# Kernel optimization log

Measured on AMD Instinct MI355X. Metric: run time of the kernel, lower is better.

The kernel has to match this reference:

```python
import jax, jax.numpy as jnp
import numpy as np

KERNEL = 3

def setup_inputs() -> dict:
    key = jax.random.key(0)
    k1, k2 = jax.random.split(key)
    x = jax.random.normal(k1, (32, 64, 64, 64), dtype=jnp.float32)
    weights = jax.random.normal(k2, (128, 64, KERNEL * KERNEL), dtype=jnp.float32)
    return {"x": x, "weights": weights}

def reference(x, weights):
    # x: (B, C, H, W); weights: (OC, C, k*k) with torch-unfold ordering
    # (channel slowest, kernel row-major) -> reshape to OIHW conv kernel.
    B, C, H, W = x.shape
    OC = weights.shape[0]
    wk = weights.reshape(OC, C, KERNEL, KERNEL)
    # stride-1, dilation-1, VALID conv == the unfold + per-(oc,c) matmul sum
    y = jax.lax.conv_general_dilated(
        x, wk, window_strides=(1, 1), padding="VALID",
        dimension_numbers=("NCHW", "OIHW", "NCHW"))
    Ho, Wo = y.shape[2], y.shape[3]
    # Faithful replication of the original's layout bug: results are laid out
    # as [oc*B + b] then reinterpreted via view(B, OC, Ho, Wo).
    y = jnp.transpose(y, (1, 0, 2, 3)).reshape(B, OC, Ho, Wo)
    return y
```

## Files before the change

kernel.cpp:

```cpp
#include <hip/hip_runtime.h>


typedef __attribute__((ext_vector_type(8))) short short8;
typedef __attribute__((ext_vector_type(4))) float f32x4;
typedef __attribute__((ext_vector_type(4))) unsigned int uint4v;

__device__ __forceinline__ unsigned short f2bf(float f) {
    unsigned u = __builtin_bit_cast(unsigned, f);
    u = (u + 0x7FFFu + ((u >> 16) & 1u)) >> 16;
    return (unsigned short)u;
}

__device__ __forceinline__ void glds16(const void* g, void* s) {
    __builtin_amdgcn_global_load_lds(
        (const __attribute__((address_space(1))) unsigned int*)g,
        (__attribute__((address_space(3))) unsigned int*)s, 16, 0, 0);
}

__global__ __launch_bounds__(256)
void transpose_x(const float* __restrict__ x, char* __restrict__ xT) {
    __shared__ float tile[64][65];
    const int tid = threadIdx.x;
    const int h = blockIdx.x, b = blockIdx.y;

    #pragma unroll
    for (int i = 0; i < 4; ++i) {
        const int idx = i * 256 + tid;
        const int c = idx >> 4, j = idx & 15;
        const float4 v = *(const float4*)(x + (size_t)(((b * 64 + c) * 64 + h) * 64 + j * 4));
        tile[c][j * 4 + 0] = v.x; tile[c][j * 4 + 1] = v.y;
        tile[c][j * 4 + 2] = v.z; tile[c][j * 4 + 3] = v.w;
    }
    __syncthreads();

    #pragma unroll
    for (int i = 0; i < 2; ++i) {
        const int idx = i * 256 + tid;
        const int col = idx >> 3, q = idx & 7;
        unsigned int wds[4];
        #pragma unroll
        for (int jj = 0; jj < 4; ++jj) {
            const unsigned short lo = f2bf(tile[q * 8 + 2 * jj + 0][col]);
            const unsigned short hi = f2bf(tile[q * 8 + 2 * jj + 1][col]);
            wds[jj] = (unsigned)lo | ((unsigned)hi << 16);
        }
        uint4v v; v[0] = wds[0]; v[1] = wds[1]; v[2] = wds[2]; v[3] = wds[3];
        *(uint4v*)(xT + (size_t)(((b * 64 + h) * 64 + col) * 128) + ((q ^ (col & 7)) * 16)) = v;
    }
}

__global__ __launch_bounds__(256)
void pack_w(const float* __restrict__ w, char* __restrict__ wT) {
    const int id = blockIdx.x * 256 + threadIdx.x;
    const int t = id >> 10;
    const int rem = id & 1023;
    const int oc = rem >> 3, q = rem & 7;
    unsigned int wds[4];
    #pragma unroll
    for (int jj = 0; jj < 4; ++jj) {
        const unsigned short lo = f2bf(w[(size_t)oc * 576 + (q * 8 + 2 * jj + 0) * 9 + t]);
        const unsigned short hi = f2bf(w[(size_t)oc * 576 + (q * 8 + 2 * jj + 1) * 9 + t]);
        wds[jj] = (unsigned)lo | ((unsigned)hi << 16);
    }
    uint4v v; v[0] = wds[0]; v[1] = wds[1]; v[2] = wds[2]; v[3] = wds[3];
    *(uint4v*)(wT + (size_t)(t * 16384 + oc * 128) + ((q ^ (oc & 7)) * 16)) = v;
}

__global__ __launch_bounds__(256, 2)
void quanv_mfma(const char* __restrict__ xT, const char* __restrict__ wT,
                float* __restrict__ out) {
    __shared__ __align__(16) char lds[65536];
    char* sx = lds;
    char* sw = lds + 49152;

    const int tid = threadIdx.x;
    const int lane = tid & 63;
    const int wid = tid >> 6;
    const int hot = blockIdx.x;
    const int b   = blockIdx.y;
    const int ho0 = hot * 4;

    for (int k = wid; k < 48; k += 4) {
        const int r = k >> 3, sub = k & 7;
        int gr = ho0 + r; if (gr > 63) gr = 63;
        glds16(xT + (size_t)((b * 64 + gr) * 8192 + sub * 1024 + lane * 16),
               sx + k * 1024);
    }
    for (int k = wid; k < 16; k += 4)
        glds16(wT + (size_t)(k * 1024 + lane * 16), sw + k * 1024);
    __syncthreads();

    const int l15 = lane & 15;
    const int quad = lane >> 4;
    const int r = wid;
    const int ho = ho0 + r;

    f32x4 acc[8][4];
    #pragma unroll
    for (int mt = 0; mt < 8; ++mt)
        #pragma unroll
        for (int nt = 0; nt < 4; ++nt)
            acc[mt][nt] = (f32x4){0.f, 0.f, 0.f, 0.f};

    #pragma unroll
    for (int tap = 0; tap < 9; ++tap) {
        const int kh = tap / 3, kw = tap % 3;

        uint4v pf[4];
        if (tap < 8) {
            #pragma unroll
            for (int i = 0; i < 4; ++i)
                pf[i] = *(const uint4v*)(wT + (size_t)((tap + 1) * 16384 +
                                                      (wid * 4 + i) * 1024 + lane * 16));
        }

        #pragma unroll
        for (int s = 0; s < 2; ++s) {
            const int q = s * 4 + quad;
            short8 a[8], bf[4];
            const int abase = l15 * 128 + ((q ^ (l15 & 7)) * 16);
            #pragma unroll
            for (int mt = 0; mt < 8; ++mt)
                a[mt] = *(const short8*)(sw + abase + mt * 2048);
            const int cb = kw + l15;
            const int bbase = (r + kh) * 8192 + cb * 128 + ((q ^ (cb & 7)) * 16);
            #pragma unroll
            for (int nt = 0; nt < 4; ++nt)
                bf[nt] = *(const short8*)(sx + bbase + nt * 2048);
            #pragma unroll
            for (int mt = 0; mt < 8; ++mt)
                #pragma unroll
                for (int nt = 0; nt < 4; ++nt)
                    acc[mt][nt] = __builtin_amdgcn_mfma_f32_16x16x32_bf16(
                        a[mt], bf[nt], acc[mt][nt], 0, 0, 0);
        }

        if (tap < 8) {
            __syncthreads();
            #pragma unroll
            for (int i = 0; i < 4; ++i)
                *(uint4v*)(sw + (wid * 4 + i) * 1024 + lane * 16) = pf[i];
            __syncthreads();
        }
    }

    if (ho < 62) {
        #pragma unroll
        for (int mt = 0; mt < 8; ++mt) {
            #pragma unroll
            for (int i = 0; i < 4; ++i) {
                const int oc = mt * 16 + quad * 4 + i;
                float* op = out + ((size_t)(oc * 32 + b) * 62 + ho) * 62;
                #pragma unroll
                for (int nt = 0; nt < 4; ++nt) {
                    const int wo = nt * 16 + l15;
                    if (wo < 62) op[wo] = acc[mt][nt][i];
                }
            }
        }
    }
}

#define CCH   8
#define OC_PT 8
#define ROWS  18
__global__ __launch_bounds__(256, 4)
void quanv_f32(const float* __restrict__ x, const float* __restrict__ w,
               float* __restrict__ out) {
    __shared__ float sx_raw[CCH * ROWS * 64 + 4];
    #define SX(cl, row, col) sx_raw[((cl) * ROWS + (row)) * 64 + (col)]
    const int tid = threadIdx.x;
    const int tx = tid & 15, ty = tid >> 4;
    const int hot = blockIdx.x, ocg = blockIdx.y, b = blockIdx.z;
    const int row0 = hot * 16, ho = row0 + ty, wo0 = tx * 4;
    const float* xb = x + (size_t)b * (64 * 64 * 64);
    const float* wb = w + (size_t)(ocg * OC_PT) * 576;
    float acc[OC_PT][4];
    #pragma unroll
    for (int o = 0; o < OC_PT; ++o)
        #pragma unroll
        for (int q = 0; q < 4; ++q) acc[o][q] = 0.f;
    for (int cc = 0; cc < 64; cc += CCH) {
        __syncthreads();
        #pragma unroll
        for (int j = 0; j < 9; ++j) {
            const int idx = j * 256 + tid;
            const int col4 = idx & 15, rowc = idx >> 4;
            const int row = rowc % ROWS, cl = rowc / ROWS;
            int gr = row0 + row; if (gr > 63) gr = 63;
            *(float4*)(&sx_raw[idx * 4]) =
                *(const float4*)(xb + ((size_t)(cc + cl) * 64 + gr) * 64 + col4 * 4);
        }
        __syncthreads();
        for (int cl = 0; cl < CCH; ++cl) {
            float xv[3][6];
            #pragma unroll
            for (int kh = 0; kh < 3; ++kh)
                #pragma unroll
                for (int j = 0; j < 6; ++j) xv[kh][j] = SX(cl, ty + kh, wo0 + j);
            const float* wc = wb + (size_t)(cc + cl) * 9;
            #pragma unroll
            for (int o = 0; o < OC_PT; ++o) {
                float wv[9];
                #pragma unroll
                for (int t = 0; t < 9; ++t) wv[t] = wc[(size_t)o * 576 + t];
                #pragma unroll
                for (int kh = 0; kh < 3; ++kh)
                    #pragma unroll
                    for (int kw = 0; kw < 3; ++kw) {
                        const float wvv = wv[kh * 3 + kw];
                        #pragma unroll
                        for (int q = 0; q < 4; ++q)
                            acc[o][q] = fmaf(xv[kh][kw + q], wvv, acc[o][q]);
                    }
            }
        }
    }
    if (ho < 62) {
        #pragma unroll
        for (int o = 0; o < OC_PT; ++o) {
            const int oc = ocg * OC_PT + o;
            float* op = out + ((size_t)(oc * 32 + b) * 62 + ho) * 62 + wo0;
            #pragma unroll
            for (int q = 0; q < 4; ++q)
                if (wo0 + q < 62) op[q] = acc[o][q];
        }
    }
    #undef SX
}

extern "C" void kernel_launch(void* const* d_in, const int* in_sizes, int n_in,
                              void* d_out, int out_size, void* d_ws, size_t ws_size,
                              hipStream_t stream) {
    const float* x = (const float*)d_in[0];
    const float* w = (const float*)d_in[1];
    float* out = (float*)d_out;

    const size_t XT_BYTES = 16777216;
    const size_t WT_BYTES = 147456;

    if (ws_size >= XT_BYTES + WT_BYTES) {
        char* xT = (char*)d_ws;
        char* wT = (char*)d_ws + XT_BYTES;
        transpose_x<<<dim3(64, 32), 256, 0, stream>>>(x, xT);
        pack_w<<<36, 256, 0, stream>>>(w, wT);
        quanv_mfma<<<dim3(16, 32), 256, 0, stream>>>(xT, wT, out);
    } else {
        quanv_f32<<<dim3(4, 16, 32), 256, 0, stream>>>(x, w, out);
    }
}
```

Before: 113.9 us.

## Double-buffer weight taps in LDS with async loads and merge prep kernels

Weight tiles for the next taps now load straight into a second LDS buffer with global_load_lds, replacing the old path that prefetched into registers, stored them to LDS and used two barriers per tap. Each tap now needs one barrier. The x-transpose and weight-pack kernels are merged into a single launch by adding an extra grid row for weight packing, which removes one kernel launch. LDS grows to 80 KB per block, so two blocks fill the CU's LDS exactly. Correctness relies on the barrier waiting for the outstanding async LDS loads before the buffer is read.

```diff
diff --git a/kernel.cpp b/kernel.cpp
--- a/kernel.cpp
+++ b/kernel.cpp
@@ -18,9 +18,30 @@
 }
 
 __global__ __launch_bounds__(256)
-void transpose_x(const float* __restrict__ x, char* __restrict__ xT) {
+void prep(const float* __restrict__ x, const float* __restrict__ w,
+          char* __restrict__ xT, char* __restrict__ wT) {
     __shared__ float tile[64][65];
     const int tid = threadIdx.x;
+
+    if (blockIdx.y == 32) {
+        const int id = blockIdx.x * 256 + tid;
+        if (id < 9216) {
+            const int t = id >> 10;
+            const int rem = id & 1023;
+            const int oc = rem >> 3, q = rem & 7;
+            unsigned int wds[4];
+            #pragma unroll
+            for (int jj = 0; jj < 4; ++jj) {
+                const unsigned short lo = f2bf(w[(size_t)oc * 576 + (q * 8 + 2 * jj + 0) * 9 + t]);
+                const unsigned short hi = f2bf(w[(size_t)oc * 576 + (q * 8 + 2 * jj + 1) * 9 + t]);
+                wds[jj] = (unsigned)lo | ((unsigned)hi << 16);
+            }
+            uint4v v; v[0] = wds[0]; v[1] = wds[1]; v[2] = wds[2]; v[3] = wds[3];
+            *(uint4v*)(wT + (size_t)(t * 16384 + oc * 128) + ((q ^ (oc & 7)) * 16)) = v;
+        }
+        return;
+    }
+
     const int h = blockIdx.x, b = blockIdx.y;
 
     #pragma unroll
@@ -49,29 +70,13 @@
     }
 }
 
-__global__ __launch_bounds__(256)
-void pack_w(const float* __restrict__ w, char* __restrict__ wT) {
-    const int id = blockIdx.x * 256 + threadIdx.x;
-    const int t = id >> 10;
-    const int rem = id & 1023;
-    const int oc = rem >> 3, q = rem & 7;
-    unsigned int wds[4];
-    #pragma unroll
-    for (int jj = 0; jj < 4; ++jj) {
-        const unsigned short lo = f2bf(w[(size_t)oc * 576 + (q * 8 + 2 * jj + 0) * 9 + t]);
-        const unsigned short hi = f2bf(w[(size_t)oc * 576 + (q * 8 + 2 * jj + 1) * 9 + t]);
-        wds[jj] = (unsigned)lo | ((unsigned)hi << 16);
-    }
-    uint4v v; v[0] = wds[0]; v[1] = wds[1]; v[2] = wds[2]; v[3] = wds[3];
-    *(uint4v*)(wT + (size_t)(t * 16384 + oc * 128) + ((q ^ (oc & 7)) * 16)) = v;
-}
-
 __global__ __launch_bounds__(256, 2)
 void quanv_mfma(const char* __restrict__ xT, const char* __restrict__ wT,
                 float* __restrict__ out) {
-    __shared__ __align__(16) char lds[65536];
-    char* sx = lds;
-    char* sw = lds + 49152;
+    __shared__ __align__(16) char lds[81920];
+    char* sx  = lds;
+    char* sw0 = lds + 49152;
+    char* sw1 = lds + 65536;
 
     const int tid = threadIdx.x;
     const int lane = tid & 63;
@@ -86,8 +91,10 @@
         glds16(xT + (size_t)((b * 64 + gr) * 8192 + sub * 1024 + lane * 16),
                sx + k * 1024);
     }
-    for (int k = wid; k < 16; k += 4)
-        glds16(wT + (size_t)(k * 1024 + lane * 16), sw + k * 1024);
+    for (int k = wid; k < 16; k += 4) {
+        glds16(wT + (size_t)(k * 1024 + lane * 16),         sw0 + k * 1024);
+        glds16(wT + (size_t)(16384 + k * 1024 + lane * 16), sw1 + k * 1024);
+    }
     __syncthreads();
 
     const int l15 = lane & 15;
@@ -105,14 +112,7 @@
     #pragma unroll
     for (int tap = 0; tap < 9; ++tap) {
         const int kh = tap / 3, kw = tap % 3;
-
-        uint4v pf[4];
-        if (tap < 8) {
-            #pragma unroll
-            for (int i = 0; i < 4; ++i)
-                pf[i] = *(const uint4v*)(wT + (size_t)((tap + 1) * 16384 +
-                                                      (wid * 4 + i) * 1024 + lane * 16));
-        }
+        char* swc = (tap & 1) ? sw1 : sw0;
 
         #pragma unroll
         for (int s = 0; s < 2; ++s) {
@@ -121,7 +121,7 @@
             const int abase = l15 * 128 + ((q ^ (l15 & 7)) * 16);
             #pragma unroll
             for (int mt = 0; mt < 8; ++mt)
-                a[mt] = *(const short8*)(sw + abase + mt * 2048);
+                a[mt] = *(const short8*)(swc + abase + mt * 2048);
             const int cb = kw + l15;
             const int bbase = (r + kh) * 8192 + cb * 128 + ((q ^ (cb & 7)) * 16);
             #pragma unroll
@@ -137,10 +137,11 @@
 
         if (tap < 8) {
             __syncthreads();
-            #pragma unroll
-            for (int i = 0; i < 4; ++i)
-                *(uint4v*)(sw + (wid * 4 + i) * 1024 + lane * 16) = pf[i];
-            __syncthreads();
+            if (tap < 7) {
+                for (int k = wid; k < 16; k += 4)
+                    glds16(wT + (size_t)((tap + 2) * 16384 + k * 1024 + lane * 16),
+                           swc + k * 1024);
+            }
         }
     }
 
@@ -242,8 +243,7 @@
     if (ws_size >= XT_BYTES + WT_BYTES) {
         char* xT = (char*)d_ws;
         char* wT = (char*)d_ws + XT_BYTES;
-        transpose_x<<<dim3(64, 32), 256, 0, stream>>>(x, xT);
-        pack_w<<<36, 256, 0, stream>>>(w, wT);
+        prep<<<dim3(64, 33), 256, 0, stream>>>(x, w, xT, wT);
         quanv_mfma<<<dim3(16, 32), 256, 0, stream>>>(xT, wT, out);
     } else {
         quanv_f32<<<dim3(4, 16, 32), 256, 0, stream>>>(x, w, out);
```

New measurement: 110.8 us. 2.7% less time.
